# Performance work log

Measured on AMD Instinct MI355X. Metric: run time of the kernel, lower is better.

Reference implementation:

```python
import jax, jax.numpy as jnp
import numpy as np

D = 512   # dim (number of groups)
H = 8192  # h = dim * v
U = 64    # u
V = H // D  # 16
N = 4096  # batch
EPS = 1e-12  # torch F.normalize eps


def setup_inputs() -> dict:
    key = jax.random.key(0)
    k_x, k_w1, k_b1, k_w2, k_b2 = jax.random.split(key, 5)
    x = jax.random.normal(k_x, (N, H), dtype=jnp.float32)
    # grouped Conv1d(dim*v, dim*u, k=1, groups=dim) == per-group [u, v] matmul
    s1 = 1.0 / np.sqrt(V)
    W1 = jax.random.uniform(k_w1, (D, U, V), jnp.float32, -s1, s1)
    b1 = jax.random.uniform(k_b1, (D, U), jnp.float32, -s1, s1)
    # grouped Conv1d(dim*u, dim, k=1, groups=dim) == per-group [1, u] matmul
    s2 = 1.0 / np.sqrt(U)
    W2 = jax.random.uniform(k_w2, (D, U), jnp.float32, -s2, s2)
    b2 = jax.random.uniform(k_b2, (D,), jnp.float32, -s2, s2)
    return {"x": x, "W1": W1, "b1": b1, "W2": W2, "b2": b2}


def reference(x, W1, b1, W2, b2):
    # x: [N, H] -> [N, D, V] (channel layout of Conv1d groups)
    xg = x.reshape(-1, D, V)
    # grouped 1x1 conv #1: per-group v -> u matmul, + bias
    h1 = jnp.einsum('ndv,duv->ndu', xg, W1) + b1  # [N, D, U]
    h1 = jax.nn.elu(h1)
    # grouped 1x1 conv #2: per-group u -> 1 matmul, + bias
    y = jnp.einsum('ndu,du->nd', h1, W2) + b2  # [N, D]
    # L2 normalize (torch F.normalize semantics: x / max(||x||, eps))
    nrm = jnp.sqrt(jnp.sum(y * y, axis=-1, keepdims=True))
    return y / jnp.maximum(nrm, EPS)
```

## Files before the change

kernel.cpp:

```cpp
#include <hip/hip_runtime.h>
#include <math.h>

#define D_ 512
#define H_ 8192
#define U_ 64
#define V_ 16
#define N_ 4096
#define DUV (D_ * U_ * V_)

#define BR 64
#define BG 8
#define YSTR 12

typedef __bf16 bf16x8 __attribute__((ext_vector_type(8)));
typedef __bf16 bf16x4 __attribute__((ext_vector_type(4)));
typedef float f32x4 __attribute__((ext_vector_type(4)));

typedef const __attribute__((address_space(1))) char* gptr_t;
typedef __attribute__((address_space(3))) char* sptr_t;

__global__ __launch_bounds__(256) void k0_split_w1(const float* __restrict__ W1,
                                                   __bf16* __restrict__ wh) {
    __bf16* wl = wh + DUV;
    const int i4 = (blockIdx.x * 256 + threadIdx.x) * 4;
    f32x4 w = *(const f32x4*)(W1 + i4);
    bf16x4 h, l;
    #pragma unroll
    for (int j = 0; j < 4; ++j) {
        float wf = w[j];
        __bf16 hh = (__bf16)wf;
        h[j] = hh;
        l[j] = (__bf16)(wf - (float)hh);
    }
    *(bf16x4*)(wh + i4) = h;
    *(bf16x4*)(wl + i4) = l;
}

template <bool PRESPLIT>
__global__ __launch_bounds__(256, 4) void k1_div_encoder(
        const float* __restrict__ x,
        const float* __restrict__ W1,
        const __bf16* __restrict__ wsplit,
        const float* __restrict__ b1,
        const float* __restrict__ W2,
        const float* __restrict__ b2,
        float* __restrict__ y) {
    __shared__ float xs[BR * 128];
    __shared__ float ytile[BR][YSTR];

    const int tid  = threadIdx.x;
    const int lane = tid & 63;
    const int wave = __builtin_amdgcn_readfirstlane(tid >> 6);
    const int q    = lane >> 4;
    const int m    = lane & 15;
    const int vbase = (q & 1) * 8;

    const int nb = blockIdx.x & 63;
    const int db = blockIdx.x >> 6;
    const int r0 = nb * BR;
    const int d0 = db * BG;

    {
        const char* gx = (const char*)(x + (size_t)r0 * H_ + (size_t)d0 * V_);
        #pragma unroll
        for (int i = 0; i < 8; ++i) {
            const int flat = tid + i * 256;
            const int row  = flat >> 5;
            const int sb   = ((flat & 31) * 16) ^ ((row & 7) << 4);
            const char* src = gx + (size_t)row * (H_ * 4) + sb;
            __builtin_amdgcn_global_load_lds((gptr_t)src,
                                             (sptr_t)((char*)xs + flat * 16),
                                             16, 0, 0);
        }
    }
    __syncthreads();

    #pragma unroll 1
    for (int gi = 0; gi < 2; ++gi) {
        const int gl = wave * 2 + gi;
        const int d  = d0 + gl;

        bf16x8 Afrag[4];
        if (PRESPLIT) {
            const __bf16* base = wsplit + (size_t)(q >> 1) * DUV;
            #pragma unroll
            for (int c = 0; c < 4; ++c) {
                Afrag[c] = *(const bf16x8*)(base +
                    ((size_t)d * U_ + c * 16 + m) * V_ + vbase);
            }
        } else {
            #pragma unroll
            for (int c = 0; c < 4; ++c) {
                const float* wp = W1 + ((size_t)d * U_ + c * 16 + m) * V_ + vbase;
                f32x4 w0 = *(const f32x4*)wp;
                f32x4 w1v = *(const f32x4*)(wp + 4);
                float wf[8] = {w0.x, w0.y, w0.z, w0.w, w1v.x, w1v.y, w1v.z, w1v.w};
                bf16x8 a;
                #pragma unroll
                for (int i = 0; i < 8; ++i) {
                    __bf16 h = (__bf16)wf[i];
                    __bf16 l = (__bf16)(wf[i] - (float)h);
                    a[i] = (q < 2) ? h : l;
                }
                Afrag[c] = a;
            }
        }

        f32x4 b1frag[4], w2frag[4];
        #pragma unroll
        for (int c = 0; c < 4; ++c) {
            b1frag[c] = *(const f32x4*)(b1 + (size_t)d * U_ + c * 16 + q * 4);
            w2frag[c] = *(const f32x4*)(W2 + (size_t)d * U_ + c * 16 + q * 4);
        }
        const float b2s = b2[d];

        #pragma unroll 2
        for (int t = 0; t < 4; ++t) {
            const int row = t * 16 + m;
            const int sw  = (row & 7) << 4;
            const char* xb = (const char*)xs + row * 512;
            f32x4 x0 = *(const f32x4*)(xb + (((gl * V_ + vbase) * 4) ^ sw));
            f32x4 x1 = *(const f32x4*)(xb + (((gl * V_ + vbase + 4) * 4) ^ sw));
            float xf[8] = {x0.x, x0.y, x0.z, x0.w, x1.x, x1.y, x1.z, x1.w};
            bf16x8 bhi, blo;
            #pragma unroll
            for (int i = 0; i < 8; ++i) {
                __bf16 h = (__bf16)xf[i];
                bhi[i] = h;
                blo[i] = (__bf16)(xf[i] - (float)h);
            }

            float partial = 0.0f;
            #pragma unroll
            for (int c = 0; c < 4; ++c) {
                f32x4 acc = b1frag[c];
                acc = __builtin_amdgcn_mfma_f32_16x16x32_bf16(Afrag[c], bhi, acc, 0, 0, 0);
                acc = __builtin_amdgcn_mfma_f32_16x16x32_bf16(Afrag[c], blo, acc, 0, 0, 0);
                #pragma unroll
                for (int r = 0; r < 4; ++r) {
                    float h = acc[r];
                    float e = fmaxf(h, __expf(fminf(h, 0.0f)) - 1.0f);
                    partial = fmaf(w2frag[c][r], e, partial);
                }
            }
            partial += __shfl_xor(partial, 16, 64);
            partial += __shfl_xor(partial, 32, 64);
            if (q == 0) {
                ytile[row][gl] = partial + b2s;
            }
        }
    }
    __syncthreads();

    if (tid < 128) {
        const int row  = tid >> 1;
        const int half = tid & 1;
        f32x4 v = *(const f32x4*)&ytile[row][half * 4];
        *(f32x4*)(y + (size_t)(r0 + row) * D_ + d0 + half * 4) = v;
    }
}

__global__ __launch_bounds__(256) void k2_l2_normalize(float* __restrict__ y) {
    const int n = blockIdx.x;
    const int t = threadIdx.x;
    float* row = y + (size_t)n * D_;

    float v0 = row[t];
    float v1 = row[t + 256];
    float ss = v0 * v0 + v1 * v1;

    #pragma unroll
    for (int off = 32; off > 0; off >>= 1) {
        ss += __shfl_down(ss, off, 64);
    }

    __shared__ float wsum[4];
    if ((t & 63) == 0) wsum[t >> 6] = ss;
    __syncthreads();
    const float tot = wsum[0] + wsum[1] + wsum[2] + wsum[3];

    const float scale = 1.0f / fmaxf(sqrtf(tot), 1e-12f);

    row[t]       = v0 * scale;
    row[t + 256] = v1 * scale;
}

extern "C" void kernel_launch(void* const* d_in, const int* in_sizes, int n_in,
                              void* d_out, int out_size, void* d_ws, size_t ws_size,
                              hipStream_t stream) {
    const float* x  = (const float*)d_in[0];
    const float* W1 = (const float*)d_in[1];
    const float* b1 = (const float*)d_in[2];
    const float* W2 = (const float*)d_in[3];
    const float* b2 = (const float*)d_in[4];
    float* y = (float*)d_out;

    const dim3 grid((N_ / BR) * (D_ / BG));
    if (ws_size >= (size_t)(2 * DUV * sizeof(__bf16))) {
        __bf16* wh = (__bf16*)d_ws;
        k0_split_w1<<<dim3(DUV / 4 / 256), dim3(256), 0, stream>>>(W1, wh);
        k1_div_encoder<true><<<grid, dim3(256), 0, stream>>>(
            x, W1, wh, b1, W2, b2, y);
    } else {
        k1_div_encoder<false><<<grid, dim3(256), 0, stream>>>(
            x, W1, (const __bf16*)nullptr, b1, W2, b2, y);
    }
    k2_l2_normalize<<<dim3(N_), dim3(256), 0, stream>>>(y);
}
```

Before: 222.9 us.

## Make encoder blocks persistent over row tiles with double-buffered LDS staging

Each block now handles 8 row tiles of a fixed group set instead of one tile. Weight fragments and biases are loaded once and kept in registers across tiles, and the next x tile is staged into a second LDS buffer while the current one is computed. The grid shrinks from 4096 to 512 blocks and launch bounds drop to 2 blocks per CU, which lowers parallelism and occupancy. There is a single barrier per iteration protecting both the x and y buffers, so correctness depends on the ordering of the async LDS loads relative to that barrier.

Result: slower. 227.5 us (+2.0%).

```diff
diff --git a/kernel.cpp b/kernel.cpp
--- a/kernel.cpp
+++ b/kernel.cpp
@@ -10,6 +10,8 @@
 
 #define BR 64
 #define BG 8
+#define NT 8
+#define CH 8
 #define YSTR 12
 
 typedef __bf16 bf16x8 __attribute__((ext_vector_type(8)));
@@ -37,7 +39,7 @@
 }
 
 template <bool PRESPLIT>
-__global__ __launch_bounds__(256, 4) void k1_div_encoder(
+__global__ __launch_bounds__(256, 2) void k1_div_encoder(
         const float* __restrict__ x,
         const float* __restrict__ W1,
         const __bf16* __restrict__ wsplit,
@@ -45,8 +47,8 @@
         const float* __restrict__ W2,
         const float* __restrict__ b2,
         float* __restrict__ y) {
-    __shared__ float xs[BR * 128];
-    __shared__ float ytile[BR][YSTR];
+    __shared__ float xs[2][BR * 128];
+    __shared__ float yt[2][BR][YSTR];
 
     const int tid  = threadIdx.x;
     const int lane = tid & 63;
@@ -55,37 +57,21 @@
     const int m    = lane & 15;
     const int vbase = (q & 1) * 8;
 
-    const int nb = blockIdx.x & 63;
-    const int db = blockIdx.x >> 6;
-    const int r0 = nb * BR;
-    const int d0 = db * BG;
-
-    {
-        const char* gx = (const char*)(x + (size_t)r0 * H_ + (size_t)d0 * V_);
-        #pragma unroll
-        for (int i = 0; i < 8; ++i) {
-            const int flat = tid + i * 256;
-            const int row  = flat >> 5;
-            const int sb   = ((flat & 31) * 16) ^ ((row & 7) << 4);
-            const char* src = gx + (size_t)row * (H_ * 4) + sb;
-            __builtin_amdgcn_global_load_lds((gptr_t)src,
-                                             (sptr_t)((char*)xs + flat * 16),
-                                             16, 0, 0);
-        }
-    }
-    __syncthreads();
-
-    #pragma unroll 1
+    const int db    = blockIdx.x >> 3;
+    const int chunk = blockIdx.x & 7;
+    const int d0    = db * BG;
+
+    bf16x8 Afrag[2][4];
+    f32x4  b1f[2][4], w2f[2][4];
+    float  b2s[2];
+    #pragma unroll
     for (int gi = 0; gi < 2; ++gi) {
-        const int gl = wave * 2 + gi;
-        const int d  = d0 + gl;
-
-        bf16x8 Afrag[4];
+        const int d = d0 + wave * 2 + gi;
         if (PRESPLIT) {
             const __bf16* base = wsplit + (size_t)(q >> 1) * DUV;
             #pragma unroll
             for (int c = 0; c < 4; ++c) {
-                Afrag[c] = *(const bf16x8*)(base +
+                Afrag[gi][c] = *(const bf16x8*)(base +
                     ((size_t)d * U_ + c * 16 + m) * V_ + vbase);
             }
         } else {
@@ -102,61 +88,90 @@
                     __bf16 l = (__bf16)(wf[i] - (float)h);
                     a[i] = (q < 2) ? h : l;
                 }
-                Afrag[c] = a;
+                Afrag[gi][c] = a;
             }
         }
-
-        f32x4 b1frag[4], w2frag[4];
         #pragma unroll
         for (int c = 0; c < 4; ++c) {
-            b1frag[c] = *(const f32x4*)(b1 + (size_t)d * U_ + c * 16 + q * 4);
-            w2frag[c] = *(const f32x4*)(W2 + (size_t)d * U_ + c * 16 + q * 4);
-        }
-        const float b2s = b2[d];
-
-        #pragma unroll 2
-        for (int t = 0; t < 4; ++t) {
-            const int row = t * 16 + m;
-            const int sw  = (row & 7) << 4;
-            const char* xb = (const char*)xs + row * 512;
-            f32x4 x0 = *(const f32x4*)(xb + (((gl * V_ + vbase) * 4) ^ sw));
-            f32x4 x1 = *(const f32x4*)(xb + (((gl * V_ + vbase + 4) * 4) ^ sw));
-            float xf[8] = {x0.x, x0.y, x0.z, x0.w, x1.x, x1.y, x1.z, x1.w};
-            bf16x8 bhi, blo;
-            #pragma unroll
-            for (int i = 0; i < 8; ++i) {
-                __bf16 h = (__bf16)xf[i];
-                bhi[i] = h;
-                blo[i] = (__bf16)(xf[i] - (float)h);
+            b1f[gi][c] = *(const f32x4*)(b1 + (size_t)d * U_ + c * 16 + q * 4);
+            w2f[gi][c] = *(const f32x4*)(W2 + (size_t)d * U_ + c * 16 + q * 4);
+        }
+        b2s[gi] = b2[d];
+    }
+
+    const int srow = tid >> 5;
+    const int sb   = ((tid & 31) * 16) ^ ((srow & 7) << 4);
+    const char* gx0 = (const char*)x
+        + (size_t)(chunk * NT * BR) * (H_ * 4) + (size_t)d0 * V_ * 4;
+
+    auto STAGE = [&](int buf, int t) {
+        const char* s = gx0 + (size_t)t * (BR * H_ * 4)
+                            + (size_t)srow * (H_ * 4) + sb;
+        char* dl = (char*)&xs[buf][0] + tid * 16;
+        #pragma unroll
+        for (int i = 0; i < 8; ++i) {
+            __builtin_amdgcn_global_load_lds((gptr_t)s, (sptr_t)dl, 16, 0, 0);
+            s  += 8 * (H_ * 4);
+            dl += 4096;
+        }
+    };
+
+    STAGE(0, 0);
+    __syncthreads();
+
+    const int sw = (m & 7) << 4;
+
+    for (int t = 0; t < NT; ++t) {
+        const int buf = t & 1;
+        if (t + 1 < NT) STAGE(buf ^ 1, t + 1);
+
+        #pragma unroll
+        for (int gi = 0; gi < 2; ++gi) {
+            const int gl = wave * 2 + gi;
+            #pragma unroll 2
+            for (int tt = 0; tt < 4; ++tt) {
+                const int row = tt * 16 + m;
+                const char* xb = (const char*)&xs[buf][0] + row * 512;
+                f32x4 x0 = *(const f32x4*)(xb + (((gl * V_ + vbase) * 4) ^ sw));
+                f32x4 x1 = *(const f32x4*)(xb + (((gl * V_ + vbase + 4) * 4) ^ sw));
+                float xf[8] = {x0.x, x0.y, x0.z, x0.w, x1.x, x1.y, x1.z, x1.w};
+                bf16x8 bhi, blo;
+                #pragma unroll
+                for (int i = 0; i < 8; ++i) {
+                    __bf16 h = (__bf16)xf[i];
+                    bhi[i] = h;
+                    blo[i] = (__bf16)(xf[i] - (float)h);
+                }
+
+                float partial = 0.0f;
+                #pragma unroll
+                for (int c = 0; c < 4; ++c) {
+                    f32x4 acc = b1f[gi][c];
+                    acc = __builtin_amdgcn_mfma_f32_16x16x32_bf16(Afrag[gi][c], bhi, acc, 0, 0, 0);
+                    acc = __builtin_amdgcn_mfma_f32_16x16x32_bf16(Afrag[gi][c], blo, acc, 0, 0, 0);
+                    #pragma unroll
+                    for (int r = 0; r < 4; ++r) {
+                        float h = acc[r];
+                        float e = fmaxf(h, __expf(fminf(h, 0.0f)) - 1.0f);
+                        partial = fmaf(w2f[gi][c][r], e, partial);
+                    }
+                }
+                partial += __shfl_xor(partial, 16, 64);
+                partial += __shfl_xor(partial, 32, 64);
+                if (q == 0) {
+                    yt[buf][row][gl] = partial + b2s[gi];
+                }
             }
-
-            float partial = 0.0f;
-            #pragma unroll
-            for (int c = 0; c < 4; ++c) {
-                f32x4 acc = b1frag[c];
-                acc = __builtin_amdgcn_mfma_f32_16x16x32_bf16(Afrag[c], bhi, acc, 0, 0, 0);
-                acc = __builtin_amdgcn_mfma_f32_16x16x32_bf16(Afrag[c], blo, acc, 0, 0, 0);
-                #pragma unroll
-                for (int r = 0; r < 4; ++r) {
-                    float h = acc[r];
-                    float e = fmaxf(h, __expf(fminf(h, 0.0f)) - 1.0f);
-                    partial = fmaf(w2frag[c][r], e, partial);
-                }
-            }
-            partial += __shfl_xor(partial, 16, 64);
-            partial += __shfl_xor(partial, 32, 64);
-            if (q == 0) {
-                ytile[row][gl] = partial + b2s;
-            }
-        }
-    }
-    __syncthreads();
-
-    if (tid < 128) {
-        const int row  = tid >> 1;
-        const int half = tid & 1;
-        f32x4 v = *(const f32x4*)&ytile[row][half * 4];
-        *(f32x4*)(y + (size_t)(r0 + row) * D_ + d0 + half * 4) = v;
+        }
+        __syncthreads();
+
+        if (tid < 128) {
+            const int row  = tid >> 1;
+            const int half = tid & 1;
+            f32x4 v = *(const f32x4*)&yt[buf][row][half * 4];
+            const int r0 = (chunk * NT + t) * BR;
+            *(f32x4*)(y + (size_t)(r0 + row) * D_ + d0 + half * 4) = v;
+        }
     }
 }
 
@@ -195,7 +210,7 @@
     const float* b2 = (const float*)d_in[4];
     float* y = (float*)d_out;
 
-    const dim3 grid((N_ / BR) * (D_ / BG));
+    const dim3 grid((D_ / BG) * CH);
     if (ws_size >= (size_t)(2 * DUV * sizeof(__bf16))) {
         __bf16* wh = (__bf16*)d_ws;
         k0_split_w1<<<dim3(DUV / 4 / 256), dim3(256), 0, stream>>>(W1, wh);
```
